# Kernel tuning notes

Hardware: AMD Instinct MI355X
Metric: run time of the kernel (lower is better)

## Reference

```python
import jax, jax.numpy as jnp
import numpy as np

B, L, D, N = 2, 2048, 1024, 16
DT = 0.1  # liquid scaler integration step


def setup_inputs() -> dict:
    key = jax.random.key(0)
    ks = jax.random.split(key, 10)
    def w(k, shape, scale=0.02):
        return jax.random.normal(k, shape, jnp.float32) * scale
    log_min, log_max = float(np.log(0.001)), float(np.log(0.1))
    dt_bias = jax.random.uniform(ks[1], (D,), jnp.float32) * (log_max - log_min) + log_min
    return {
        "x": jax.random.normal(ks[0], (B, L, D), jnp.float32),
        "delta_W": w(ks[2], (D, D)), "delta_b": jnp.zeros((D,), jnp.float32),
        "B_W": w(ks[3], (N, D)), "B_b": jnp.zeros((N,), jnp.float32),
        "C_W": w(ks[4], (N, D)), "C_b": jnp.zeros((N,), jnp.float32),
        "A_log": jnp.zeros((D, N), jnp.float32),
        "dt_bias": dt_bias,
        "tau": jnp.ones((N,), jnp.float32),
        "Wi_W": w(ks[5], (N, D)), "Wi_b": jnp.zeros((N,), jnp.float32),
        "Wr_W": w(ks[6], (N, N)),
        "sel_W": w(ks[7], (D, N)), "sel_b": jnp.zeros((D,), jnp.float32),
        "h0": jnp.zeros((1, N), jnp.float32),
    }


def reference(x, delta_W, delta_b, B_W, B_b, C_W, C_b, A_log, dt_bias, tau,
              Wi_W, Wi_b, Wr_W, sel_W, sel_b, h0):
    Bsz, Ls, Dm = x.shape
    Ns = A_log.shape[1]

    # --- LiquidTimeConstantScaler ---
    gc = x.mean(axis=1)                                # [B, D]
    inp_sig = gc @ Wi_W.T + Wi_b                       # [B, N]
    cur = jnp.broadcast_to(h0, (Bsz, Ns))              # [B, N]
    rec = cur @ Wr_W.T                                 # [B, N]
    tau_c = jnp.clip(tau, 0.1, 10.0)
    dh_dt = (-cur + jnp.tanh(inp_sig + rec)) / tau_c[None, :]
    new_h = cur + DT * dh_dt                           # [B, N]
    sel = jax.nn.sigmoid(new_h @ sel_W.T + sel_b)      # [B, D]
    xs = x * sel[:, None, :]                           # [B, L, D]

    # --- selective SSM discretization ---
    delta = jax.nn.softplus(xs @ delta_W.T + delta_b + dt_bias)  # [B, L, D]
    Bm = xs @ B_W.T + B_b                              # [B, L, N]
    Cm = xs @ C_W.T + C_b                              # [B, L, N]
    A = -jnp.exp(A_log)                                # [D, N]
    A_d = jnp.exp(A[None, None] * delta[..., None])    # [B, L, D, N]
    factor = jnp.where(jnp.abs(A)[None, None] < 1e-6,
                       delta[..., None], (A_d - 1.0) / A[None, None])
    B_d = factor * Bm[:, :, None, :]                   # [B, L, D, N]

    # --- linear recurrence over time via scan ---
    def step(h, inputs):
        Ad_t, Bd_t, x_t, C_t = inputs                  # [B,D,N],[B,D,N],[B,D],[B,N]
        h = Ad_t * h + Bd_t * x_t[..., None]
        y = jnp.einsum('bdn,bn->bd', h, C_t)
        return h, y

    h_init = jnp.zeros((Bsz, Dm, Ns), x.dtype)
    _, ys = jax.lax.scan(step, h_init,
                         (A_d.transpose(1, 0, 2, 3), B_d.transpose(1, 0, 2, 3),
                          xs.transpose(1, 0, 2), Cm.transpose(1, 0, 2)))
    return ys.transpose(1, 0, 2)                        # [B, L, D]
```

## Files before the change

kernel.cpp:

```cpp
#include <hip/hip_runtime.h>
#include <hip/hip_bf16.h>
#include <math.h>

#define B_ 2
#define L_ 2048
#define D_ 1024
#define N_ 16
#define CCH 64
#define TCH 32
#define NCOLS 1056
#define NPAD  1088

typedef unsigned short u16;
typedef __attribute__((ext_vector_type(8))) short short8v;
typedef __attribute__((ext_vector_type(8))) unsigned short ushort8v;
typedef __attribute__((ext_vector_type(4))) float f32x4;

__device__ __forceinline__ float softplusf(float z) {
  return fmaxf(z, 0.f) + log1pf(__expf(-fabsf(z)));
}

__device__ __forceinline__ u16 bf16rne(float f) {
  union { float f; unsigned u; } c; c.f = f;
  unsigned u = c.u;
  u += 0x7fffu + ((u >> 16) & 1u);
  return (u16)(u >> 16);
}

__device__ __forceinline__ float bf16tof(u16 v) {
  union { unsigned u; float f; } c;
  c.u = (unsigned)v << 16;
  return c.f;
}

__device__ __forceinline__ void gl_lds16(const void* g, const u16* lds_base,
                                         int byte_off) {
  byte_off = __builtin_amdgcn_readfirstlane(byte_off);
  __builtin_amdgcn_global_load_lds(
      (const __attribute__((address_space(1))) void*)g,
      (__attribute__((address_space(3))) void*)((const char*)lds_base + byte_off),
      16, 0, 0);
}

__global__ __launch_bounds__(256) void k_gc_pack(const float* __restrict__ x,
    float* __restrict__ part1, u16* __restrict__ xb) {
  int blk = blockIdx.x;
  int b = blk >> 8, lc = blk & 255;
  int tid = threadIdx.x;
  int r0 = b * L_ + lc * 8;
  float4 s = {0.f, 0.f, 0.f, 0.f};
  #pragma unroll
  for (int q = 0; q < 8; ++q) {
    size_t off = (size_t)(r0 + q) * D_ + tid * 4;
    float4 v = *(const float4*)(x + off);
    s.x += v.x; s.y += v.y; s.z += v.z; s.w += v.w;
    ushort4 r;
    r.x = bf16rne(v.x); r.y = bf16rne(v.y);
    r.z = bf16rne(v.z); r.w = bf16rne(v.w);
    *(ushort4*)(xb + off) = r;
  }
  *(float4*)(part1 + (size_t)blk * D_ + tid * 4) = s;
}

__global__ __launch_bounds__(256) void k_gc_red(const float* __restrict__ part1,
                                                float* __restrict__ part2) {
  int gid = blockIdx.x * 256 + threadIdx.x;
  int d = gid & 1023;
  int jc = (gid >> 10) & 15;
  int b = gid >> 14;
  float s = 0.f;
  #pragma unroll
  for (int t = 0; t < 16; ++t)
    s += part1[(size_t)(b * 256 + jc * 16 + t) * D_ + d];
  part2[gid] = s;
}

__global__ __launch_bounds__(256) void k_newh_sel(const float* __restrict__ part2,
    const float* __restrict__ Wi_W, const float* __restrict__ Wi_b,
    const float* __restrict__ Wr_W, const float* __restrict__ tau,
    const float* __restrict__ h0, const float* __restrict__ sel_W,
    const float* __restrict__ sel_b, float* __restrict__ selp) {
  __shared__ float gcs[B_ * D_];
  __shared__ float nh[B_ * N_];
  int tid = threadIdx.x;
  for (int idx = tid; idx < B_ * D_; idx += 256) {
    int b = idx >> 10, d = idx & (D_ - 1);
    float s = 0.f;
    #pragma unroll
    for (int lc = 0; lc < 16; ++lc)
      s += part2[(size_t)((b << 4) | lc) * D_ + d];
    gcs[idx] = s * (1.f / L_);
  }
  __syncthreads();
  if (tid < B_ * N_) {
    int b = tid >> 4, n = tid & 15;
    float inp = Wi_b[n];
    const float* g = gcs + b * D_;
    const float* w = Wi_W + n * D_;
    for (int d = 0; d < D_; d += 4) {
      float4 gv = *(const float4*)(g + d);
      float4 wv = *(const float4*)(w + d);
      inp += gv.x * wv.x + gv.y * wv.y + gv.z * wv.z + gv.w * wv.w;
    }
    float rec = 0.f;
    for (int m = 0; m < N_; ++m) rec += h0[m] * Wr_W[n * N_ + m];
    float th = tanhf(inp + rec);
    float tc = fminf(fmaxf(tau[n], 0.1f), 10.f);
    float cur = h0[n];
    nh[tid] = cur + 0.1f * ((th - cur) / tc);
  }
  __syncthreads();
  for (int i = tid; i < B_ * D_; i += 256) {
    int b = i >> 10, d = i & (D_ - 1);
    const float* w = sel_W + d * N_;
    const float* h = nh + b * N_;
    float z = sel_b[d];
    #pragma unroll
    for (int n = 0; n < N_; n += 4) {
      float4 wv = *(const float4*)(w + n);
      z += h[n] * wv.x + h[n + 1] * wv.y + h[n + 2] * wv.z + h[n + 3] * wv.w;
    }
    selp[i] = 1.f / (1.f + __expf(-z));
  }
}

__global__ __launch_bounds__(256) void k_pack_w(const float* __restrict__ dW,
    const float* __restrict__ B_W, const float* __restrict__ C_W,
    const float* __restrict__ sel, u16* __restrict__ Wp) {
  int gid = blockIdx.x * 256 + threadIdx.x;
  int b = blockIdx.y;
  size_t e = (size_t)gid * 8;
  int nn = (int)(e >> 10);
  int k = (int)(e & 1023);
  ushort8v r;
  if (nn < NCOLS) {
    const float* src = (nn < 1024) ? dW + (size_t)nn * 1024
                     : (nn < 1040) ? B_W + (size_t)(nn - 1024) * 1024
                                   : C_W + (size_t)(nn - 1040) * 1024;
    float4 s0 = *(const float4*)(src + k);
    float4 s1 = *(const float4*)(src + k + 4);
    const float* sp = sel + b * D_ + k;
    float4 e0 = *(const float4*)sp;
    float4 e1 = *(const float4*)(sp + 4);
    r[0] = bf16rne(s0.x * e0.x); r[1] = bf16rne(s0.y * e0.y);
    r[2] = bf16rne(s0.z * e0.z); r[3] = bf16rne(s0.w * e0.w);
    r[4] = bf16rne(s1.x * e1.x); r[5] = bf16rne(s1.y * e1.y);
    r[6] = bf16rne(s1.z * e1.z); r[7] = bf16rne(s1.w * e1.w);
  } else {
    r = (ushort8v)0;
  }
  *(ushort8v*)(Wp + (size_t)b * (NPAD * 1024) + e) = r;
}

__global__ __launch_bounds__(256) void k_gemm(
    const u16* __restrict__ xb, const u16* __restrict__ Wp,
    const float* __restrict__ delta_b, const float* __restrict__ dt_bias,
    const float* __restrict__ B_b, const float* __restrict__ C_b,
    float* __restrict__ delta, float* __restrict__ Bm, float* __restrict__ Cm) {
  __shared__ __align__(16) u16 lds[6][4096];
  int m0 = blockIdx.x * 64;
  int n0 = blockIdx.y * 64;
  int batch = blockIdx.x >> 5;
  const u16* wb = Wp + (size_t)batch * (NPAD * 1024);
  int tid = threadIdx.x;
  int w = tid >> 6, l = tid & 63;
  int wr = w >> 1, wc = w & 1;
  int srow = l >> 3;
  int ssl = (l & 7) ^ srow;

  f32x4 acc[2][2];
  #pragma unroll
  for (int m = 0; m < 2; ++m)
    #pragma unroll
    for (int n = 0; n < 2; ++n)
      acc[m][n] = (f32x4){0.f, 0.f, 0.f, 0.f};

  #define STAGE(kb, buf)                                                       \
    {                                                                          \
      _Pragma("unroll")                                                        \
      for (int q = 0; q < 2; ++q) {                                            \
        int row = w * 16 + q * 8 + srow;                                       \
        gl_lds16(xb + (size_t)(m0 + row) * 1024 + (kb) * 64 + ssl * 8,         \
                 &lds[0][0], (buf) * 8192 + (w * 16 + q * 8) * 128);           \
        gl_lds16(wb + (size_t)(n0 + row) * 1024 + (kb) * 64 + ssl * 8,         \
                 &lds[0][0], 24576 + (buf) * 8192 + (w * 16 + q * 8) * 128);   \
      }                                                                        \
    }

  int lr = l & 15, lh = l >> 4;

  #define CSTEP(cur)                                                           \
    {                                                                          \
      _Pragma("unroll")                                                        \
      for (int ks = 0; ks < 2; ++ks) {                                         \
        short8v a[2], bq[2];                                                   \
        _Pragma("unroll")                                                      \
        for (int m = 0; m < 2; ++m) {                                          \
          int r = wr * 32 + m * 16 + lr;                                       \
          int ps = (ks * 4 + lh) ^ (r & 7);                                    \
          a[m] = *(const short8v*)((const char*)&lds[0][0] + (cur) * 8192 + r * 128 + ps * 16);\
        }                                                                      \
        _Pragma("unroll")                                                      \
        for (int n = 0; n < 2; ++n) {                                          \
          int r = wc * 32 + n * 16 + lr;                                       \
          int ps = (ks * 4 + lh) ^ (r & 7);                                    \
          bq[n] = *(const short8v*)((const char*)&lds[0][0] + 24576 + (cur) * 8192 + r * 128 + ps * 16);\
        }                                                                      \
        _Pragma("unroll")                                                      \
        for (int m = 0; m < 2; ++m)                                            \
          _Pragma("unroll")                                                    \
          for (int n = 0; n < 2; ++n)                                          \
            acc[m][n] = __builtin_amdgcn_mfma_f32_16x16x32_bf16(a[m], bq[n],   \
                                                                acc[m][n], 0, 0, 0);\
      }                                                                        \
    }

  STAGE(0, 0);
  STAGE(1, 1);
  #pragma unroll
  for (int kb = 0; kb < 14; ++kb) {
    STAGE(kb + 2, (kb + 2) % 3);
    asm volatile("s_waitcnt vmcnt(8)" ::: "memory");
    __builtin_amdgcn_s_barrier();
    CSTEP(kb % 3);
    asm volatile("s_waitcnt lgkmcnt(0)" ::: "memory");
    __builtin_amdgcn_s_barrier();
  }
  asm volatile("s_waitcnt vmcnt(4)" ::: "memory");
  __builtin_amdgcn_s_barrier();
  CSTEP(2);
  asm volatile("s_waitcnt lgkmcnt(0)" ::: "memory");
  __builtin_amdgcn_s_barrier();
  asm volatile("s_waitcnt vmcnt(0)" ::: "memory");
  __builtin_amdgcn_s_barrier();
  CSTEP(0);
  #undef STAGE
  #undef CSTEP

  int ibase = m0 + wr * 32 + lh * 4;
  int jbase = n0 + wc * 32 + lr;
  #pragma unroll
  for (int m = 0; m < 2; ++m) {
    #pragma unroll
    for (int n = 0; n < 2; ++n) {
      int j = jbase + n * 16;
      #pragma unroll
      for (int r = 0; r < 2 * 2; ++r) {
        int i = ibase + m * 16 + r;
        float v = acc[m][n][r];
        if (j < 1024) {
          delta[(size_t)i * D_ + j] = softplusf(v + delta_b[j] + dt_bias[j]);
        } else if (j < 1040) {
          Bm[i * N_ + (j - 1024)] = v + B_b[j - 1024];
        } else if (j < NCOLS) {
          Cm[i * N_ + (j - 1040)] = v + C_b[j - 1040];
        }
      }
    }
  }
}

__global__ __launch_bounds__(256) void k_scan1(const u16* __restrict__ xb,
    const float* __restrict__ sel, const float* __restrict__ delta,
    const float* __restrict__ Bm, const float* __restrict__ A_log,
    float* __restrict__ prodA, float* __restrict__ hend) {
  int gid = blockIdx.x * 256 + threadIdx.x;
  int nq = gid & 3;
  int d = (gid >> 2) & (D_ - 1);
  int c = (gid >> 12) & (CCH - 1);
  int b = gid >> 18;
  float A[4], rA[4];
  unsigned smallm = 0;
  {
    float4 a0 = *(const float4*)(A_log + d * N_ + nq * 4);
    float av[4] = {a0.x, a0.y, a0.z, a0.w};
    #pragma unroll
    for (int n = 0; n < 4; ++n) {
      float a = -__expf(av[n]);
      A[n] = a; rA[n] = 1.f / a;
      if (fabsf(a) < 1e-6f) smallm |= (1u << n);
    }
  }
  float selv = sel[b * D_ + d];
  float h[4], p[4];
  #pragma unroll
  for (int n = 0; n < 4; ++n) { h[n] = 0.f; p[n] = 1.f; }
  int row0 = b * L_ + c * TCH;
  const u16* xp = xb + (size_t)row0 * D_ + d;
  const float* dp = delta + (size_t)row0 * D_ + d;
  const float4* bmp = (const float4*)(Bm + (size_t)row0 * N_) + nq;
  #pragma unroll 4
  for (int s = 0; s < TCH; ++s) {
    float dlt = dp[(size_t)s * D_];
    float xv = bf16tof(xp[(size_t)s * D_]) * selv;
    float4 q0 = bmp[s * 4];
    float bmv[4] = {q0.x, q0.y, q0.z, q0.w};
    #pragma unroll
    for (int n = 0; n < 4; ++n) {
      float Ad = __expf(A[n] * dlt);
      float f = ((smallm >> n) & 1u) ? dlt : (Ad - 1.f) * rA[n];
      h[n] = Ad * h[n] + (f * bmv[n]) * xv;
      p[n] *= Ad;
    }
  }
  size_t base = ((size_t)(gid >> 2)) * N_ + nq * 4;
  *(float4*)(prodA + base) = make_float4(p[0], p[1], p[2], p[3]);
  *(float4*)(hend + base)  = make_float4(h[0], h[1], h[2], h[3]);
}

__global__ __launch_bounds__(256) void k_scan2(const float* __restrict__ prodA,
    const float* __restrict__ hend, float* __restrict__ hin) {
  int gid = blockIdx.x * 256 + threadIdx.x;
  int b = gid >> 14;
  int rem = gid & 16383;
  size_t base = ((size_t)(b * CCH) << 14) + rem;
  float H = 0.f;
  #pragma unroll
  for (int g = 0; g < 4; ++g) {
    float pg[16], hg[16];
    #pragma unroll
    for (int t = 0; t < 16; ++t) {
      size_t idx = base + ((size_t)(g * 16 + t) << 14);
      pg[t] = prodA[idx];
      hg[t] = hend[idx];
    }
    #pragma unroll
    for (int t = 0; t < 16; ++t) {
      size_t idx = base + ((size_t)(g * 16 + t) << 14);
      hin[idx] = H;
      H = pg[t] * H + hg[t];
    }
  }
}

__global__ __launch_bounds__(256) void k_scan3(const u16* __restrict__ xb,
    const float* __restrict__ sel, const float* __restrict__ delta,
    const float* __restrict__ Bm, const float* __restrict__ Cm,
    const float* __restrict__ A_log, const float* __restrict__ hin,
    float* __restrict__ out) {
  int gid = blockIdx.x * 256 + threadIdx.x;
  int nq = gid & 3;
  int d = (gid >> 2) & (D_ - 1);
  int c = (gid >> 12) & (CCH - 1);
  int b = gid >> 18;
  float A[4], rA[4];
  unsigned smallm = 0;
  {
    float4 a0 = *(const float4*)(A_log + d * N_ + nq * 4);
    float av[4] = {a0.x, a0.y, a0.z, a0.w};
    #pragma unroll
    for (int n = 0; n < 4; ++n) {
      float a = -__expf(av[n]);
      A[n] = a; rA[n] = 1.f / a;
      if (fabsf(a) < 1e-6f) smallm |= (1u << n);
    }
  }
  float selv = sel[b * D_ + d];
  float h[4];
  {
    size_t base = ((size_t)(gid >> 2)) * N_ + nq * 4;
    float4 v0 = *(const float4*)(hin + base);
    h[0] = v0.x; h[1] = v0.y; h[2] = v0.z; h[3] = v0.w;
  }
  int row0 = b * L_ + c * TCH;
  const u16* xp = xb + (size_t)row0 * D_ + d;
  const float* dp = delta + (size_t)row0 * D_ + d;
  const float4* bmp = (const float4*)(Bm + (size_t)row0 * N_) + nq;
  const float4* cmp = (const float4*)(Cm + (size_t)row0 * N_) + nq;
  float* op = out + (size_t)row0 * D_ + d;
  #pragma unroll 4
  for (int s = 0; s < TCH; ++s) {
    float dlt = dp[(size_t)s * D_];
    float xv = bf16tof(xp[(size_t)s * D_]) * selv;
    float4 q0 = bmp[s * 4];
    float4 r0 = cmp[s * 4];
    float bmv[4] = {q0.x, q0.y, q0.z, q0.w};
    float cmv[4] = {r0.x, r0.y, r0.z, r0.w};
    float yp = 0.f;
    #pragma unroll
    for (int n = 0; n < 4; ++n) {
      float Ad = __expf(A[n] * dlt);
      float f = ((smallm >> n) & 1u) ? dlt : (Ad - 1.f) * rA[n];
      h[n] = Ad * h[n] + (f * bmv[n]) * xv;
      yp += h[n] * cmv[n];
    }
    float y = yp + __shfl_xor(yp, 1, 64);
    y += __shfl_xor(y, 2, 64);
    if (nq == 0) op[(size_t)s * D_] = y;
  }
}

extern "C" void kernel_launch(void* const* d_in, const int* in_sizes, int n_in,
                              void* d_out, int out_size, void* d_ws, size_t ws_size,
                              hipStream_t stream) {
  const float* x       = (const float*)d_in[0];
  const float* deltaW  = (const float*)d_in[1];
  const float* deltab  = (const float*)d_in[2];
  const float* B_W     = (const float*)d_in[3];
  const float* B_b     = (const float*)d_in[4];
  const float* C_W     = (const float*)d_in[5];
  const float* C_b     = (const float*)d_in[6];
  const float* A_log   = (const float*)d_in[7];
  const float* dt_bias = (const float*)d_in[8];
  const float* tau     = (const float*)d_in[9];
  const float* Wi_W    = (const float*)d_in[10];
  const float* Wi_b    = (const float*)d_in[11];
  const float* Wr_W    = (const float*)d_in[12];
  const float* sel_W   = (const float*)d_in[13];
  const float* sel_b   = (const float*)d_in[14];
  const float* h0      = (const float*)d_in[15];
  float* out = (float*)d_out;

  float* ws    = (float*)d_ws;
  float* delta = ws;
  float* selp  = delta + 4194304;
  float* Bm    = selp + 2048;
  float* Cm    = Bm + 65536;
  u16*   xb    = (u16*)(Cm + 65536);
  u16*   Wp    = xb + 4194304;
  float* hin   = (float*)(Wp + 2228224);
  float* part1 = hin;
  float* part2 = hin + 524288;
  float* prodA = out;
  float* hend  = out + 2097152;

  hipLaunchKernelGGL(k_gc_pack, dim3(512), dim3(256), 0, stream, x, part1, xb);
  hipLaunchKernelGGL(k_gc_red, dim3(128), dim3(256), 0, stream, part1, part2);
  hipLaunchKernelGGL(k_newh_sel, dim3(1), dim3(256), 0, stream,
                     part2, Wi_W, Wi_b, Wr_W, tau, h0, sel_W, sel_b, selp);
  hipLaunchKernelGGL(k_pack_w, dim3(544, 2), dim3(256), 0, stream,
                     deltaW, B_W, C_W, selp, Wp);
  hipLaunchKernelGGL(k_gemm, dim3(64, 17), dim3(256), 0, stream,
                     xb, Wp, deltab, dt_bias, B_b, C_b, delta, Bm, Cm);
  hipLaunchKernelGGL(k_scan1, dim3(2048), dim3(256), 0, stream,
                     xb, selp, delta, Bm, A_log, prodA, hend);
  hipLaunchKernelGGL(k_scan2, dim3(128), dim3(256), 0, stream,
                     prodA, hend, hin);
  hipLaunchKernelGGL(k_scan3, dim3(2048), dim3(256), 0, stream,
                     xb, selp, delta, Bm, Cm, A_log, hin, out);
}
```

Measured before the change: 131.5 us.

## Give each wave a private LDS region and drop block barriers in GEMM

Each wave in the projection GEMM now stages its own 32 rows of A and 32 rows of B into a private LDS slice, with double buffering instead of a shared triple buffer. This removes all s_barrier calls from the main loop, and LDS fragment reads are split from the MFMA issue so the next stage load can overlap with the MFMAs. The cost is redundant global loads, since each A and B tile row is now fetched by two waves instead of one. LDS use grows to 64KB, which may lower occupancy.

```diff
diff --git a/kernel.cpp b/kernel.cpp
--- a/kernel.cpp
+++ b/kernel.cpp
@@ -157,7 +157,7 @@
     const float* __restrict__ delta_b, const float* __restrict__ dt_bias,
     const float* __restrict__ B_b, const float* __restrict__ C_b,
     float* __restrict__ delta, float* __restrict__ Bm, float* __restrict__ Cm) {
-  __shared__ __align__(16) u16 lds[6][4096];
+  __shared__ __align__(16) u16 lds[32768];
   int m0 = blockIdx.x * 64;
   int n0 = blockIdx.y * 64;
   int batch = blockIdx.x >> 5;
@@ -167,6 +167,7 @@
   int wr = w >> 1, wc = w & 1;
   int srow = l >> 3;
   int ssl = (l & 7) ^ srow;
+  int wbase = w * 16384;
 
   f32x4 acc[2][2];
   #pragma unroll
@@ -178,64 +179,76 @@
   #define STAGE(kb, buf)                                                       \
     {                                                                          \
       _Pragma("unroll")                                                        \
-      for (int q = 0; q < 2; ++q) {                                            \
-        int row = w * 16 + q * 8 + srow;                                       \
-        gl_lds16(xb + (size_t)(m0 + row) * 1024 + (kb) * 64 + ssl * 8,         \
-                 &lds[0][0], (buf) * 8192 + (w * 16 + q * 8) * 128);           \
-        gl_lds16(wb + (size_t)(n0 + row) * 1024 + (kb) * 64 + ssl * 8,         \
-                 &lds[0][0], 24576 + (buf) * 8192 + (w * 16 + q * 8) * 128);   \
+      for (int q = 0; q < 4; ++q) {                                            \
+        int ra = m0 + wr * 32 + q * 8 + srow;                                  \
+        gl_lds16(xb + (size_t)ra * 1024 + (kb) * 64 + ssl * 8,                 \
+                 &lds[0], wbase + (buf) * 8192 + q * 1024);                    \
+        int rb = n0 + wc * 32 + q * 8 + srow;                                  \
+        gl_lds16(wb + (size_t)rb * 1024 + (kb) * 64 + ssl * 8,                 \
+                 &lds[0], wbase + (buf) * 8192 + 4096 + q * 1024);             \
       }                                                                        \
     }
 
   int lr = l & 15, lh = l >> 4;
-
-  #define CSTEP(cur)                                                           \
+  short8v a_[2][2], b_[2][2];
+
+  #define CSTEP_READ(buf)                                                      \
     {                                                                          \
       _Pragma("unroll")                                                        \
       for (int ks = 0; ks < 2; ++ks) {                                         \
-        short8v a[2], bq[2];                                                   \
         _Pragma("unroll")                                                      \
         for (int m = 0; m < 2; ++m) {                                          \
-          int r = wr * 32 + m * 16 + lr;                                       \
+          int r = m * 16 + lr;                                                 \
           int ps = (ks * 4 + lh) ^ (r & 7);                                    \
-          a[m] = *(const short8v*)((const char*)&lds[0][0] + (cur) * 8192 + r * 128 + ps * 16);\
+          a_[ks][m] = *(const short8v*)((const char*)&lds[0] + wbase +         \
+                                        (buf) * 8192 + r * 128 + ps * 16);     \
         }                                                                      \
         _Pragma("unroll")                                                      \
         for (int n = 0; n < 2; ++n) {                                          \
-          int r = wc * 32 + n * 16 + lr;                                       \
+          int r = n * 16 + lr;                                                 \
           int ps = (ks * 4 + lh) ^ (r & 7);                                    \
-          bq[n] = *(const short8v*)((const char*)&lds[0][0] + 24576 + (cur) * 8192 + r * 128 + ps * 16);\
+          b_[ks][n] = *(const short8v*)((const char*)&lds[0] + wbase +         \
+                                        (buf) * 8192 + 4096 + r * 128 + ps * 16);\
         }                                                                      \
+      }                                                                        \
+    }
+
+  #define CSTEP_MFMA()                                                         \
+    {                                                                          \
+      _Pragma("unroll")                                                        \
+      for (int ks = 0; ks < 2; ++ks)                                           \
         _Pragma("unroll")                                                      \
         for (int m = 0; m < 2; ++m)                                            \
           _Pragma("unroll")                                                    \
           for (int n = 0; n < 2; ++n)                                          \
-            acc[m][n] = __builtin_amdgcn_mfma_f32_16x16x32_bf16(a[m], bq[n],   \
-                                                                acc[m][n], 0, 0, 0);\
-      }                                                                        \
+            acc[m][n] = __builtin_amdgcn_mfma_f32_16x16x32_bf16(               \
+                a_[ks][m], b_[ks][n], acc[m][n], 0, 0, 0);                     \
     }
 
   STAGE(0, 0);
   STAGE(1, 1);
   #pragma unroll
   for (int kb = 0; kb < 14; ++kb) {
-    STAGE(kb + 2, (kb + 2) % 3);
     asm volatile("s_waitcnt vmcnt(8)" ::: "memory");
-    __builtin_amdgcn_s_barrier();
-    CSTEP(kb % 3);
+    CSTEP_READ(kb & 1);
     asm volatile("s_waitcnt lgkmcnt(0)" ::: "memory");
-    __builtin_amdgcn_s_barrier();
-  }
-  asm volatile("s_waitcnt vmcnt(4)" ::: "memory");
-  __builtin_amdgcn_s_barrier();
-  CSTEP(2);
+    __builtin_amdgcn_sched_barrier(0);
+    STAGE(kb + 2, kb & 1);
+    CSTEP_MFMA();
+  }
+  asm volatile("s_waitcnt vmcnt(8)" ::: "memory");
+  CSTEP_READ(0);
   asm volatile("s_waitcnt lgkmcnt(0)" ::: "memory");
-  __builtin_amdgcn_s_barrier();
+  __builtin_amdgcn_sched_barrier(0);
+  CSTEP_MFMA();
   asm volatile("s_waitcnt vmcnt(0)" ::: "memory");
-  __builtin_amdgcn_s_barrier();
-  CSTEP(0);
+  CSTEP_READ(1);
+  asm volatile("s_waitcnt lgkmcnt(0)" ::: "memory");
+  __builtin_amdgcn_sched_barrier(0);
+  CSTEP_MFMA();
   #undef STAGE
-  #undef CSTEP
+  #undef CSTEP_READ
+  #undef CSTEP_MFMA
 
   int ibase = m0 + wr * 32 + lh * 4;
   int jbase = n0 + wc * 32 + lr;
@@ -245,7 +258,7 @@
     for (int n = 0; n < 2; ++n) {
       int j = jbase + n * 16;
       #pragma unroll
-      for (int r = 0; r < 2 * 2; ++r) {
+      for (int r = 0; r < 4; ++r) {
         int i = ibase + m * 16 + r;
         float v = acc[m][n][r];
         if (j < 1024) {
```

Result: slower. 139.3 us (+5.9%).
